# Performance work log

Measured on AMD Instinct MI355X. Metric: run time of the kernel, lower is better.

## Reference

```python
import jax, jax.numpy as jnp
import numpy as np

E = 8
D_IN = 1024
D_HID = 4096
D_OUT = 1024
T = 16384  # total tokens, equally split: 2048 per expert


def setup_inputs() -> dict:
    key = jax.random.key(0)
    k1, k2, k3, k4, k5 = jax.random.split(key, 5)
    x = jax.random.normal(k1, (T, D_IN), dtype=jnp.float32)
    cnt = jnp.full((E,), T // E, dtype=jnp.int32)  # tokens per expert (sorted/contiguous)
    s1 = 1.0 / np.sqrt(D_IN)
    s2 = 1.0 / np.sqrt(D_HID)
    w1 = jax.random.uniform(k2, (E, D_HID, D_IN), jnp.float32, -s1, s1)
    b1 = jax.random.uniform(k3, (E, D_HID), jnp.float32, -s1, s1)
    w2 = jax.random.uniform(k4, (E, D_OUT, D_HID), jnp.float32, -s2, s2)
    b2 = jax.random.uniform(k5, (E, D_OUT), jnp.float32, -s2, s2)
    return {"x": x, "cnt": cnt, "w1": w1, "b1": b1, "w2": w2, "b2": b2}


def reference(x, cnt, w1, b1, w2, b2):
    # FMoELinear: tokens are laid out contiguously by expert per `cnt`.
    # With equal counts (T // E per expert) the grouped GEMM is a batched einsum.
    e = w1.shape[0]
    t, d = x.shape
    cap = t // e  # tokens per expert
    xg = x.reshape(e, cap, d)                               # [E, cap, d_in]
    h = jnp.einsum('ecd,ehd->ech', xg, w1) + b1[:, None, :]  # fc1: [E, cap, d_hid]
    h = jax.nn.gelu(h, approximate=False)                    # nn.GELU (exact erf)
    # drop1 / drop2 are p=0.0 (identity); sub_norm is Identity (use_subln=False)
    y = jnp.einsum('ech,eoh->eco', h, w2) + b2[:, None, :]   # fc2: [E, cap, d_out]
    return y.reshape(t, -1)
```

## Files before the change

kernel.cpp:

```cpp
#include <hip/hip_runtime.h>
#include <hip/hip_bf16.h>
#include <cstdint>

#define NUM_E 8
#define DIN   1024
#define DHID  4096
#define DOUTP 1024
#define TTOK  16384
#define CAP   2048

typedef __attribute__((ext_vector_type(8))) short bf16x8;
typedef __attribute__((ext_vector_type(4))) float f32x4;

static __device__ __forceinline__ ushort f32_to_bf16_rne(float f) {
  uint32_t b = __float_as_uint(f);
  b += 0x7fffu + ((b >> 16) & 1u);
  return (ushort)(b >> 16);
}

static __device__ __forceinline__ float erf_fast(float x) {
  const float ax = __builtin_fabsf(x);
  const float t  = __builtin_amdgcn_rcpf(__builtin_fmaf(0.3275911f, ax, 1.0f));
  float p = __builtin_fmaf(1.061405429f, t, -1.453152027f);
  p = __builtin_fmaf(p, t, 1.421413741f);
  p = __builtin_fmaf(p, t, -0.284496736f);
  p = __builtin_fmaf(p, t, 0.254829592f);
  p = p * t;
  const float e = __expf(-ax * ax);
  const float r = __builtin_fmaf(-p, e, 1.0f);
  return __builtin_copysignf(r, x);
}

__global__ void __launch_bounds__(256) cvt_bf16_kernel(const float* __restrict__ in,
                                                       ushort* __restrict__ out,
                                                       unsigned n) {
  unsigned i = (blockIdx.x * 256u + threadIdx.x) * 8u;
  const unsigned stride = gridDim.x * 256u * 8u;
  for (; i < n; i += stride) {
    float4 a = *reinterpret_cast<const float4*>(in + i);
    float4 b = *reinterpret_cast<const float4*>(in + i + 4);
    union { ushort u[8]; uint4 v; } o;
    o.u[0] = f32_to_bf16_rne(a.x); o.u[1] = f32_to_bf16_rne(a.y);
    o.u[2] = f32_to_bf16_rne(a.z); o.u[3] = f32_to_bf16_rne(a.w);
    o.u[4] = f32_to_bf16_rne(b.x); o.u[5] = f32_to_bf16_rne(b.y);
    o.u[6] = f32_to_bf16_rne(b.z); o.u[7] = f32_to_bf16_rne(b.w);
    *reinterpret_cast<uint4*>(out + i) = o.v;
  }
}

#define GLD(g, l)                                                                 \
  __builtin_amdgcn_global_load_lds((const __attribute__((address_space(1))) void*)(g), \
                                   (__attribute__((address_space(3))) void*)(l), 16, 0, 0)

template <int K, int N, int TILES_N, bool GELU_BF16_OUT>
__global__ void __launch_bounds__(512, 1) grouped_gemm_kernel(
    const ushort* __restrict__ A,
    const ushort* __restrict__ B,
    const float* __restrict__ bias,
    void* __restrict__ Cout) {
  constexpr int TILES_M = CAP / 256;
  constexpr int BPE = TILES_M * TILES_N;
  constexpr int NT = K / 64;
  constexpr int NTI = NT / 2;
  static_assert(NT >= 4 && (NT & 1) == 0, "need even NT >= 4");

  __shared__ uint8_t lds[131072];

  const int tid = (blockIdx.x & 7) * BPE + (blockIdx.x >> 3);
  const int e   = tid / BPE;
  const int rm  = tid % BPE;
  const int nt  = rm / TILES_M;
  const int mt  = rm % TILES_M;

  const int t  = threadIdx.x;
  const int w  = t >> 6, l = t & 63;
  const int wm = w >> 2, wn = w & 3;
  const int lr = l & 15;
  const int kg = l >> 4;
  const int col0 = nt * 256 + wn * 64;

  const int gr  = t >> 3;
  const int sch = (t & 7) ^ (gr & 7);
  const ushort* gA = A + ((long)(e * CAP + mt * 256) + gr) * K + sch * 8;
  const ushort* gB = B + ((long)(e * N) + nt * 256 + gr) * K + sch * 8;
  uint8_t* const dT = lds + t * 16;

#define SA(j, h) { const ushort* s_ = gA + (long)(h) * 128 * K + (long)(j) * 64;   \
    uint8_t* d_ = dT + (((j) & 1) << 16) + ((h) << 14);                            \
    GLD(s_, d_); GLD(s_ + (long)64 * K, d_ + 8192); }
#define SB(j, h) { const ushort* s_ = gB + (long)(h) * 128 * K + (long)(j) * 64;   \
    uint8_t* d_ = dT + (((j) & 1) << 16) + 32768 + ((h) << 14);                    \
    GLD(s_, d_); GLD(s_ + (long)64 * K, d_ + 8192); }

  int offA[8][2], offB[4][2];
#pragma unroll
  for (int m = 0; m < 8; ++m) {
    const int r = m * 16 + lr;
#pragma unroll
    for (int kh = 0; kh < 2; ++kh)
      offA[m][kh] = r * 128 + ((((kh << 2) | kg) ^ (r & 7)) << 4);
  }
#pragma unroll
  for (int n = 0; n < 4; ++n) {
    const int r = (wn & 1) * 64 + n * 16 + lr;
#pragma unroll
    for (int kh = 0; kh < 2; ++kh)
      offB[n][kh] = r * 128 + ((((kh << 2) | kg) ^ (r & 7)) << 4);
  }
  const int rdAoff = wm << 14;
  const int rdBoff = 32768 + ((wn >> 1) << 14);

  f32x4 acc[8][4] = {};

  SA(0, 0); SA(0, 1); SB(0, 0); SB(0, 1);
  SB(1, 0); SB(1, 1);
  asm volatile("s_waitcnt vmcnt(4)" ::: "memory");
  __builtin_amdgcn_s_barrier();

#define PHASE_MFMA(AF, BF, AI, NI)                                                 \
    __builtin_amdgcn_s_barrier();                                                  \
    asm volatile("s_waitcnt lgkmcnt(0)" ::: "memory");                             \
    __builtin_amdgcn_sched_barrier(0);                                             \
    __builtin_amdgcn_s_setprio(1);                                                 \
    _Pragma("unroll")                                                              \
    for (int m = 0; m < 4; ++m)                                                    \
      _Pragma("unroll")                                                            \
      for (int n = 0; n < 2; ++n)                                                  \
        _Pragma("unroll")                                                          \
        for (int kh = 0; kh < 2; ++kh)                                             \
          acc[m + (AI)][n + (NI)] = __builtin_amdgcn_mfma_f32_16x16x32_bf16(       \
              AF[m][kh], BF[n][kh], acc[m + (AI)][n + (NI)], 0, 0, 0);             \
    __builtin_amdgcn_s_setprio(0);

#define RD_A0(SRC) _Pragma("unroll")                                               \
    for (int m = 0; m < 4; ++m) _Pragma("unroll")                                  \
      for (int kh = 0; kh < 2; ++kh)                                               \
        a0[m][kh] = *reinterpret_cast<const bf16x8*>((SRC) + offA[m][kh]);
#define RD_A1(SRC) _Pragma("unroll")                                               \
    for (int m = 0; m < 4; ++m) _Pragma("unroll")                                  \
      for (int kh = 0; kh < 2; ++kh)                                               \
        a1[m][kh] = *reinterpret_cast<const bf16x8*>((SRC) + offA[m + 4][kh]);
#define RD_B0(SRC) _Pragma("unroll")                                               \
    for (int n = 0; n < 2; ++n) _Pragma("unroll")                                  \
      for (int kh = 0; kh < 2; ++kh)                                               \
        b0[n][kh] = *reinterpret_cast<const bf16x8*>((SRC) + offB[n][kh]);
#define RD_B1(SRC) _Pragma("unroll")                                               \
    for (int n = 0; n < 2; ++n) _Pragma("unroll")                                  \
      for (int kh = 0; kh < 2; ++kh)                                               \
        b1[n][kh] = *reinterpret_cast<const bf16x8*>((SRC) + offB[n + 2][kh]);

  for (int i = 0; i < NTI; ++i) {
    const int u = 2 * i, v = u + 1;
    const bool st = (u + 2) < NT;
    const uint8_t* rA0 = lds + rdAoff;
    const uint8_t* rB0 = lds + rdBoff;
    const uint8_t* rA1 = lds + 65536 + rdAoff;
    const uint8_t* rB1 = lds + 65536 + rdBoff;
    bf16x8 a0[4][2], a1[4][2], b0[2][2], b1[2][2];

    RD_A0(rA0) RD_B0(rB0)
    SA(v, 0);
    PHASE_MFMA(a0, b0, 0, 0)
    __builtin_amdgcn_s_barrier();

    RD_B1(rB0)
    SA(v, 1);
    PHASE_MFMA(a0, b1, 0, 2)
    __builtin_amdgcn_s_barrier();

    RD_A1(rA0)
    if (st) SB(u + 2, 0);
    PHASE_MFMA(a1, b1, 4, 2)
    __builtin_amdgcn_s_barrier();

    if (st) SB(u + 2, 1);
    PHASE_MFMA(a1, b0, 4, 0)
    if (st) { asm volatile("s_waitcnt vmcnt(4)" ::: "memory"); }
    else    { asm volatile("s_waitcnt vmcnt(0)" ::: "memory"); }
    __builtin_amdgcn_s_barrier();

    RD_A0(rA1) RD_B0(rB1)
    if (st) SA(u + 2, 0);
    PHASE_MFMA(a0, b0, 0, 0)
    __builtin_amdgcn_s_barrier();

    RD_B1(rB1)
    if (st) SA(u + 2, 1);
    PHASE_MFMA(a0, b1, 0, 2)
    __builtin_amdgcn_s_barrier();

    RD_A1(rA1)
    if (st) SB(v + 2, 0);
    PHASE_MFMA(a1, b1, 4, 2)
    __builtin_amdgcn_s_barrier();

    if (st) SB(v + 2, 1);
    PHASE_MFMA(a1, b0, 4, 0)
    if (st) { asm volatile("s_waitcnt vmcnt(4)" ::: "memory"); }
    __builtin_amdgcn_s_barrier();
  }

  const long rowg0 = (long)e * CAP + mt * 256 + wm * 128;
  float bv[4];
#pragma unroll
  for (int n = 0; n < 4; ++n) bv[n] = bias[(long)e * N + col0 + n * 16 + lr];

  if constexpr (GELU_BF16_OUT) {
    uint8_t* const sl = lds + (w << 14);
#pragma unroll
    for (int n = 0; n < 4; ++n) {
#pragma unroll
      for (int m = 0; m < 8; ++m) {
#pragma unroll
        for (int q = 0; q < 4; ++q) {
          const int r = m * 16 + kg * 4 + q;
          const int c = n * 16 + lr;
          float vx = acc[m][n][q] + bv[n];
          vx = 0.5f * vx * (1.0f + erf_fast(vx * 0.70710678118654752f));
          *(ushort*)(sl + r * 128 + ((((c >> 3) ^ (r & 7))) << 4) + (c & 7) * 2) =
              f32_to_bf16_rne(vx);
        }
      }
    }
    asm volatile("s_waitcnt lgkmcnt(0)" ::: "memory");
    ushort* const Cb = (ushort*)Cout;
#pragma unroll
    for (int it = 0; it < 16; ++it) {
      const int idx = it * 64 + l;
      const int r = idx >> 3, c16 = idx & 7;
      uint4 vv = *reinterpret_cast<const uint4*>(sl + r * 128 + ((c16 ^ (r & 7)) << 4));
      *reinterpret_cast<uint4*>(Cb + (rowg0 + r) * N + col0 + c16 * 8) = vv;
    }
  } else {
    float* const Cf = (float*)Cout;
#pragma unroll
    for (int n = 0; n < 4; ++n) {
#pragma unroll
      for (int m = 0; m < 8; ++m) {
#pragma unroll
        for (int q = 0; q < 4; ++q) {
          const int r = m * 16 + kg * 4 + q;
          Cf[(rowg0 + r) * N + col0 + n * 16 + lr] = acc[m][n][q] + bv[n];
        }
      }
    }
  }
#undef SA
#undef SB
#undef PHASE_MFMA
#undef RD_A0
#undef RD_A1
#undef RD_B0
#undef RD_B1
}

extern "C" void kernel_launch(void* const* d_in, const int* in_sizes, int n_in,
                              void* d_out, int out_size, void* d_ws, size_t ws_size,
                              hipStream_t stream) {
  const float* x  = (const float*)d_in[0];
  const float* w1 = (const float*)d_in[2];
  const float* b1 = (const float*)d_in[3];
  const float* w2 = (const float*)d_in[4];
  const float* b2 = (const float*)d_in[5];
  float* out = (float*)d_out;

  constexpr size_t W2B_OFF = 67108864;
  constexpr size_t HB_OFF  = 134217728;
  constexpr size_t WS_NEED = 268435456;
  if (ws_size < WS_NEED) return;

  ushort* w1b = (ushort*)d_ws;
  ushort* w2b = (ushort*)d_ws + W2B_OFF;
  ushort* hb  = (ushort*)d_ws + HB_OFF;
  ushort* xb  = (ushort*)d_out;

  cvt_bf16_kernel<<<2048, 256, 0, stream>>>(x,  xb,  (unsigned)(TTOK * DIN));
  cvt_bf16_kernel<<<2048, 256, 0, stream>>>(w1, w1b, (unsigned)(NUM_E * DHID * DIN));
  cvt_bf16_kernel<<<2048, 256, 0, stream>>>(w2, w2b, (unsigned)(NUM_E * DOUTP * DHID));

  grouped_gemm_kernel<DIN, DHID, DHID / 256, true>
      <<<dim3(NUM_E * (CAP / 256) * (DHID / 256)), 512, 0, stream>>>(xb, w1b, b1, hb);

  grouped_gemm_kernel<DHID, DOUTP, DOUTP / 256, false>
      <<<dim3(NUM_E * (CAP / 256) * (DOUTP / 256)), 512, 0, stream>>>(hb, w2b, b2, out);
}
```

Baseline: 375.5 us.

## Merge x/w1 conversions into one launch and fold w2 conversion into fc1 epilogue

Replaces three separate fp32-to-bf16 conversion launches with one kernel that converts both x and w1. The w2 conversion moves into the tail of the fc1 GEMM, where each block converts a fixed 32768-element slice after its epilogue. This removes launch overhead and tries to hide the memory-bound w2 conversion behind compute-bound GEMM blocks. The cost is a longer tail per fc1 block and extra memory traffic competing with the GEMM.

```diff
diff --git a/kernel.cpp b/kernel.cpp
--- a/kernel.cpp
+++ b/kernel.cpp
@@ -31,33 +31,40 @@
   return __builtin_copysignf(r, x);
 }
 
-__global__ void __launch_bounds__(256) cvt_bf16_kernel(const float* __restrict__ in,
-                                                       ushort* __restrict__ out,
-                                                       unsigned n) {
-  unsigned i = (blockIdx.x * 256u + threadIdx.x) * 8u;
+static __device__ __forceinline__ void cvt8(const float* __restrict__ in,
+                                            ushort* __restrict__ out) {
+  float4 a = *reinterpret_cast<const float4*>(in);
+  float4 b = *reinterpret_cast<const float4*>(in + 4);
+  union { ushort u[8]; uint4 v; } o;
+  o.u[0] = f32_to_bf16_rne(a.x); o.u[1] = f32_to_bf16_rne(a.y);
+  o.u[2] = f32_to_bf16_rne(a.z); o.u[3] = f32_to_bf16_rne(a.w);
+  o.u[4] = f32_to_bf16_rne(b.x); o.u[5] = f32_to_bf16_rne(b.y);
+  o.u[6] = f32_to_bf16_rne(b.z); o.u[7] = f32_to_bf16_rne(b.w);
+  *reinterpret_cast<uint4*>(out) = o.v;
+}
+
+__global__ void __launch_bounds__(256) cvt2_bf16_kernel(
+    const float* __restrict__ in1, ushort* __restrict__ out1, unsigned n1,
+    const float* __restrict__ in2, ushort* __restrict__ out2, unsigned n2) {
   const unsigned stride = gridDim.x * 256u * 8u;
-  for (; i < n; i += stride) {
-    float4 a = *reinterpret_cast<const float4*>(in + i);
-    float4 b = *reinterpret_cast<const float4*>(in + i + 4);
-    union { ushort u[8]; uint4 v; } o;
-    o.u[0] = f32_to_bf16_rne(a.x); o.u[1] = f32_to_bf16_rne(a.y);
-    o.u[2] = f32_to_bf16_rne(a.z); o.u[3] = f32_to_bf16_rne(a.w);
-    o.u[4] = f32_to_bf16_rne(b.x); o.u[5] = f32_to_bf16_rne(b.y);
-    o.u[6] = f32_to_bf16_rne(b.z); o.u[7] = f32_to_bf16_rne(b.w);
-    *reinterpret_cast<uint4*>(out + i) = o.v;
-  }
+  for (unsigned i = (blockIdx.x * 256u + threadIdx.x) * 8u; i < n1; i += stride)
+    cvt8(in1 + i, out1 + i);
+  for (unsigned i = (blockIdx.x * 256u + threadIdx.x) * 8u; i < n2; i += stride)
+    cvt8(in2 + i, out2 + i);
 }
 
 #define GLD(g, l)                                                                 \
   __builtin_amdgcn_global_load_lds((const __attribute__((address_space(1))) void*)(g), \
                                    (__attribute__((address_space(3))) void*)(l), 16, 0, 0)
 
-template <int K, int N, int TILES_N, bool GELU_BF16_OUT>
+template <int K, int N, int TILES_N, bool GELU_BF16_OUT, bool CVT_W2>
 __global__ void __launch_bounds__(512, 1) grouped_gemm_kernel(
     const ushort* __restrict__ A,
     const ushort* __restrict__ B,
     const float* __restrict__ bias,
-    void* __restrict__ Cout) {
+    void* __restrict__ Cout,
+    const float* __restrict__ cvt_src,
+    ushort* __restrict__ cvt_dst) {
   constexpr int TILES_M = CAP / 256;
   constexpr int BPE = TILES_M * TILES_N;
   constexpr int NT = K / 64;
@@ -245,6 +252,15 @@
       }
     }
   }
+
+  if constexpr (CVT_W2) {
+    const long base = (long)blockIdx.x * 32768;
+#pragma unroll
+    for (int it = 0; it < 8; ++it) {
+      const long idx = base + (long)it * 4096 + t * 8;
+      cvt8(cvt_src + idx, cvt_dst + idx);
+    }
+  }
 #undef SA
 #undef SB
 #undef PHASE_MFMA
@@ -274,13 +290,14 @@
   ushort* hb  = (ushort*)d_ws + HB_OFF;
   ushort* xb  = (ushort*)d_out;
 
-  cvt_bf16_kernel<<<2048, 256, 0, stream>>>(x,  xb,  (unsigned)(TTOK * DIN));
-  cvt_bf16_kernel<<<2048, 256, 0, stream>>>(w1, w1b, (unsigned)(NUM_E * DHID * DIN));
-  cvt_bf16_kernel<<<2048, 256, 0, stream>>>(w2, w2b, (unsigned)(NUM_E * DOUTP * DHID));
-
-  grouped_gemm_kernel<DIN, DHID, DHID / 256, true>
-      <<<dim3(NUM_E * (CAP / 256) * (DHID / 256)), 512, 0, stream>>>(xb, w1b, b1, hb);
-
-  grouped_gemm_kernel<DHID, DOUTP, DOUTP / 256, false>
-      <<<dim3(NUM_E * (CAP / 256) * (DOUTP / 256)), 512, 0, stream>>>(hb, w2b, b2, out);
-}
+  cvt2_bf16_kernel<<<2048, 256, 0, stream>>>(
+      x, xb, (unsigned)(TTOK * DIN), w1, w1b, (unsigned)(NUM_E * DHID * DIN));
+
+  grouped_gemm_kernel<DIN, DHID, DHID / 256, true, true>
+      <<<dim3(NUM_E * (CAP / 256) * (DHID / 256)), 512, 0, stream>>>(
+          xb, w1b, b1, hb, w2, w2b);
+
+  grouped_gemm_kernel<DHID, DOUTP, DOUTP / 256, false, false>
+      <<<dim3(NUM_E * (CAP / 256) * (DOUTP / 256)), 512, 0, stream>>>(
+          hb, w2b, b2, out, nullptr, nullptr);
+}
```

After: 353.2 us, median of 2. 5.9% less time.
